# Performance work log

Hardware: AMD Instinct MI355X
Metric: run time of the kernel (lower is better)

Reference implementation:

```python
import jax, jax.numpy as jnp
import numpy as np

DIM = 4096
N_HEADS = 32
N_KV_HEADS = 8
HEAD_DIM = DIM // N_HEADS  # 128
N_REP = N_HEADS // N_KV_HEADS  # 4
FFN_HIDDEN = 11008
EPS = 1e-6
B, S = 4, 2048


def rms_norm(x, gamma):
    # x: [b, s, d]
    var = jnp.mean(x * x, axis=-1, keepdims=True)
    return gamma * (x * jax.lax.rsqrt(var + EPS))


def apply_rope(x, cos, sin):
    # x: [b, s, h, d]; cos/sin: [s, d/2]. Complex rotation on (even, odd) pairs.
    x2 = x.reshape(*x.shape[:-1], HEAD_DIM // 2, 2)
    x0, x1 = x2[..., 0], x2[..., 1]
    c = cos[None, :, None, :]
    s = sin[None, :, None, :]
    r0 = x0 * c - x1 * s
    r1 = x0 * s + x1 * c
    return jnp.stack([r0, r1], axis=-1).reshape(x.shape)


def setup_inputs() -> dict:
    key = jax.random.key(0)
    ks = jax.random.split(key, 16)
    sc = 0.02
    inp = {
        "x": jax.random.normal(ks[0], (B, S, DIM), dtype=jnp.float32),
        "freqs": jax.random.uniform(ks[1], (S, HEAD_DIM // 2), dtype=jnp.float32) * (2 * np.pi),
        "start_pos": 0,
        "gamma_attn": jnp.ones((DIM,), jnp.float32),
        "gamma_ffn": jnp.ones((DIM,), jnp.float32),
        "wq_w": sc * jax.random.normal(ks[2], (N_HEADS * HEAD_DIM, DIM), jnp.float32),
        "wq_b": jnp.zeros((N_HEADS * HEAD_DIM,), jnp.float32),
        "wk_w": sc * jax.random.normal(ks[3], (N_KV_HEADS * HEAD_DIM, DIM), jnp.float32),
        "wk_b": jnp.zeros((N_KV_HEADS * HEAD_DIM,), jnp.float32),
        "wv_w": sc * jax.random.normal(ks[4], (N_KV_HEADS * HEAD_DIM, DIM), jnp.float32),
        "wv_b": jnp.zeros((N_KV_HEADS * HEAD_DIM,), jnp.float32),
        "wo_w": sc * jax.random.normal(ks[5], (DIM, N_HEADS * HEAD_DIM), jnp.float32),
        "wo_b": jnp.zeros((DIM,), jnp.float32),
        "w1_w": sc * jax.random.normal(ks[6], (FFN_HIDDEN, DIM), jnp.float32),
        "w3_w": sc * jax.random.normal(ks[7], (FFN_HIDDEN, DIM), jnp.float32),
        "w2_w": sc * jax.random.normal(ks[8], (DIM, FFN_HIDDEN), jnp.float32),
    }
    return inp


def reference(x, freqs, start_pos, gamma_attn, gamma_ffn,
              wq_w, wq_b, wk_w, wk_b, wv_w, wv_b, wo_w, wo_b,
              w1_w, w3_w, w2_w):
    cos, sin = jnp.cos(freqs), jnp.sin(freqs)

    # --- attention sublayer ---
    xn = rms_norm(x, gamma_attn)
    xq = (xn @ wq_w.T + wq_b).reshape(B, S, N_HEADS, HEAD_DIM)
    xk = (xn @ wk_w.T + wk_b).reshape(B, S, N_KV_HEADS, HEAD_DIM)
    xv = (xn @ wv_w.T + wv_b).reshape(B, S, N_KV_HEADS, HEAD_DIM)
    xq = apply_rope(xq, cos, sin)
    xk = apply_rope(xk, cos, sin)

    # KV cache: start_pos=0 prefill -> cache slice [0:start_pos+S] == current xk/xv
    keys = jnp.repeat(xk, N_REP, axis=2)   # [b, s, n_heads, d]
    values = jnp.repeat(xv, N_REP, axis=2)

    scores = jnp.einsum('bqhd,bkhd->bhqk', xq, keys) / np.sqrt(HEAD_DIM)
    probs = jax.nn.softmax(scores.astype(jnp.float32), axis=-1).astype(xq.dtype)
    attn = jnp.einsum('bhqk,bkhd->bqhd', probs, values).reshape(B, S, DIM)
    h = x + attn @ wo_w.T + wo_b

    # --- FFN sublayer (LLaMA SwiGLU) ---
    hn = rms_norm(h, gamma_ffn)
    ff = (jax.nn.silu(hn @ w1_w.T) * (hn @ w3_w.T)) @ w2_w.T
    return h + ff
```

## Files before the change

### kernel.cpp

```cpp
#include <hip/hip_runtime.h>
#include <hip/hip_bf16.h>

#define DIM   4096
#define NH    32
#define NKV   8
#define HD    128
#define FFNH  11008
#define BATCH 4
#define SEQ   2048
#define MTOT  (BATCH*SEQ)

using bf16x8_t = __attribute__((ext_vector_type(8))) short;
using f32x4_t  = __attribute__((ext_vector_type(4))) float;

typedef const __attribute__((address_space(1))) unsigned int GlbU32;
typedef __attribute__((address_space(3))) unsigned int LdsU32;

__device__ __forceinline__ unsigned short f2b(float f) {
  union { float f; unsigned int u; } v; v.f = f;
  return (unsigned short)((v.u + 0x7fffu + ((v.u >> 16) & 1u)) >> 16);
}
__device__ __forceinline__ float b2f(unsigned short b) {
  union { unsigned int u; float f; } v; v.u = ((unsigned int)b) << 16;
  return v.f;
}
__device__ __forceinline__ void gll16(const void* g, void* l) {
  __builtin_amdgcn_global_load_lds((GlbU32*)g, (LdsU32*)l, 16, 0, 0);
}

#define VM8  asm volatile("s_waitcnt vmcnt(8)" ::: "memory")
#define VM4M asm volatile("s_waitcnt vmcnt(4)" ::: "memory")
#define VM0  asm volatile("s_waitcnt vmcnt(0)" ::: "memory")

__global__ __launch_bounds__(256)
void cvt_bf16_k(const float* __restrict__ src, unsigned short* __restrict__ dst)
{
  const size_t i = ((size_t)blockIdx.x * 256 + threadIdx.x) * 8;
  const float4 a = *(const float4*)&src[i];
  const float4 b = *(const float4*)&src[i + 4];
  union { int4 v; unsigned short u[8]; } o;
  o.u[0] = f2b(a.x); o.u[1] = f2b(a.y); o.u[2] = f2b(a.z); o.u[3] = f2b(a.w);
  o.u[4] = f2b(b.x); o.u[5] = f2b(b.y); o.u[6] = f2b(b.z); o.u[7] = f2b(b.w);
  *(int4*)&dst[i] = o.v;
}

__global__ __launch_bounds__(256)
void rmsnorm_k(const float* __restrict__ X, const float* __restrict__ gamma,
               unsigned short* __restrict__ Y)
{
  const int row = blockIdx.x, t = threadIdx.x;
  const float* xr = X + (size_t)row * DIM;
  float4 v[4];
  float ss = 0.f;
#pragma unroll
  for (int p = 0; p < 4; ++p) {
    v[p] = *(const float4*)&xr[p * 1024 + t * 4];
    ss += v[p].x*v[p].x + v[p].y*v[p].y + v[p].z*v[p].z + v[p].w*v[p].w;
  }
#pragma unroll
  for (int off = 32; off >= 1; off >>= 1) ss += __shfl_xor(ss, off, 64);
  __shared__ float red[4];
  if ((t & 63) == 0) red[t >> 6] = ss;
  __syncthreads();
  const float tot = red[0] + red[1] + red[2] + red[3];
  const float rn = rsqrtf(tot * (1.f / DIM) + 1e-6f);
  unsigned short* yr = Y + (size_t)row * DIM;
#pragma unroll
  for (int p = 0; p < 4; ++p) {
    const float4 gv = *(const float4*)&gamma[p * 1024 + t * 4];
    short4 o;
    o.x = (short)f2b(v[p].x * gv.x * rn);
    o.y = (short)f2b(v[p].y * gv.y * rn);
    o.z = (short)f2b(v[p].z * gv.z * rn);
    o.w = (short)f2b(v[p].w * gv.w * rn);
    *(short4*)&yr[p * 1024 + t * 4] = o;
  }
}

template<int NHT>
__global__ __launch_bounds__(256)
void rope_k(unsigned short* __restrict__ buf, const float* __restrict__ fr)
{
  const int u = blockIdx.x * 256 + threadIdx.x;
  const int per_row = NHT * 16;
  const int row  = u / per_row;
  const int rem  = u - row * per_row;
  const int head = rem >> 4;
  const int i4   = (rem & 15) << 2;
  const int s    = row & (SEQ - 1);
  unsigned short* p = buf + (size_t)row * (NHT * HD) + head * HD + i4 * 2;
  union { int4 v; unsigned short u16[8]; } d;
  d.v = *(const int4*)p;
  const float4 f = *(const float4*)&fr[s * 64 + i4];
  const float fa[4] = {f.x, f.y, f.z, f.w};
#pragma unroll
  for (int i = 0; i < 4; ++i) {
    float sn, c;
    __sincosf(fa[i], &sn, &c);
    const float x0 = b2f(d.u16[2*i]), x1 = b2f(d.u16[2*i+1]);
    d.u16[2*i]   = f2b(x0 * c - x1 * sn);
    d.u16[2*i+1] = f2b(x0 * sn + x1 * c);
  }
  *(int4*)p = d.v;
}

#define GP0(SLOT, STG, VM) {                                              \
  _Pragma("unroll") for (int n_ = 0; n_ < 4; ++n_) bf[n_] = rdB((SLOT), n_); \
  _Pragma("unroll") for (int m_ = 0; m_ < 4; ++m_) af[m_] = rdA((SLOT), m_ * 16); \
  STG;                                                                    \
  __builtin_amdgcn_s_barrier();                                           \
  asm volatile("s_waitcnt lgkmcnt(0)" ::: "memory");                      \
  __builtin_amdgcn_sched_barrier(0);                                      \
  __builtin_amdgcn_s_setprio(1);                                          \
  _Pragma("unroll") for (int m_ = 0; m_ < 4; ++m_)                        \
    _Pragma("unroll") for (int n_ = 0; n_ < 4; ++n_)                      \
      acc[m_][n_] = __builtin_amdgcn_mfma_f32_16x16x32_bf16(af[m_], bf[n_], acc[m_][n_], 0, 0, 0); \
  __builtin_amdgcn_s_setprio(0);                                          \
  VM;                                                                     \
  __builtin_amdgcn_s_barrier();                                           \
  __builtin_amdgcn_sched_barrier(0);                                      \
}
#define GP1(SLOT, STG, VM) {                                              \
  _Pragma("unroll") for (int m_ = 0; m_ < 4; ++m_) af[m_] = rdA((SLOT), 64 + m_ * 16); \
  STG;                                                                    \
  __builtin_amdgcn_s_barrier();                                           \
  asm volatile("s_waitcnt lgkmcnt(0)" ::: "memory");                      \
  __builtin_amdgcn_sched_barrier(0);                                      \
  __builtin_amdgcn_s_setprio(1);                                          \
  _Pragma("unroll") for (int m_ = 0; m_ < 4; ++m_)                        \
    _Pragma("unroll") for (int n_ = 0; n_ < 4; ++n_)                      \
      acc[4 + m_][n_] = __builtin_amdgcn_mfma_f32_16x16x32_bf16(af[m_], bf[n_], acc[4 + m_][n_], 0, 0, 0); \
  __builtin_amdgcn_s_setprio(0);                                          \
  VM;                                                                     \
  __builtin_amdgcn_s_barrier();                                           \
  __builtin_amdgcn_sched_barrier(0);                                      \
}

template<int MODE>
__global__ __launch_bounds__(512)
void gemm256(const unsigned short* __restrict__ A,
             const unsigned short* __restrict__ W,
             const unsigned short* __restrict__ W3p,
             const float* __restrict__ bias,
             const float* res,
             float* outF,
             unsigned short* __restrict__ outH,
             const unsigned short* __restrict__ wkp,
             const unsigned short* __restrict__ wvp,
             const float* __restrict__ bkp,
             const float* __restrict__ bvp,
             unsigned short* __restrict__ okp,
             unsigned short* __restrict__ ovp,
             int K)
{
  __shared__ __align__(16) char smem[131072];
  const int t = threadIdx.x, lane = t & 63, wid = t >> 6;
  const int wr = wid >> 2, wc = wid & 3;
  const int G = gridDim.x, bid = blockIdx.x;
  const int wg = (bid & 7) * (G >> 3) + (bid >> 3);
  const int NBN = G >> 5;
  const int span = NBN << 3;
  const int tmg = wg / span, rr = wg - tmg * span;
  const int tn = rr >> 3, tm = (tmg << 3) + (rr & 7);
  const int m0 = tm << 8;
  const int NT = K >> 6, NSUB = K >> 5;

  const unsigned short *P1, *P2;
  const float* bp = bias;
  unsigned short* oh = outH;
  int nloc = 0, colsN = 4096;
  if constexpr (MODE == 0) {
    const int n0 = tn << 8;
    if (n0 < 4096)      { nloc = n0;        P1 = W   + (size_t)nloc * K; bp = bias; oh = outH; colsN = 4096; }
    else if (n0 < 5120) { nloc = n0 - 4096; P1 = wkp + (size_t)nloc * K; bp = bkp;  oh = okp;  colsN = 1024; }
    else                { nloc = n0 - 5120; P1 = wvp + (size_t)nloc * K; bp = bvp;  oh = ovp;  colsN = 1024; }
    P2 = P1 + (size_t)128 * K;
  } else if constexpr (MODE == 3) {
    const int n0w = tn << 7;
    P1 = W   + (size_t)n0w * K;
    P2 = W3p + (size_t)n0w * K;
    nloc = n0w;
  } else {
    const int n0 = tn << 8;
    P1 = W + (size_t)n0 * K;
    P2 = P1 + (size_t)128 * K;
    nloc = n0;
  }

  const int r0 = t >> 2, gg = t & 3;
  const int gsw = gg ^ ((r0 >> 1) & 3);

  auto stA = [&](int sig) {
    if (sig < NSUB) {
      const int slot = sig & 3;
      gll16(A + (size_t)(m0 + r0) * K + sig * 32 + gsw * 8,
            smem + slot * 16384 + wid * 1024);
      gll16(A + (size_t)(m0 + 128 + r0) * K + sig * 32 + gsw * 8,
            smem + slot * 16384 + 8192 + wid * 1024);
    }
  };
  auto stB = [&](int sig) {
    if (sig < NSUB) {
      const int slot = sig & 3;
      gll16(P1 + (size_t)r0 * K + sig * 32 + gsw * 8,
            smem + 65536 + slot * 16384 + wid * 1024);
      gll16(P2 + (size_t)r0 * K + sig * 32 + gsw * 8,
            smem + 65536 + slot * 16384 + 8192 + wid * 1024);
    }
  };
  auto rdA = [&](int slot, int mo) -> bf16x8_t {
    const int lrow = wr * 128 + mo + (lane & 15);
    const int g = (lane >> 4) ^ ((lrow >> 1) & 3);
    return *(const bf16x8_t*)(smem + slot * 16384 + lrow * 64 + g * 16);
  };
  auto rdB = [&](int slot, int nf) -> bf16x8_t {
    const int brow = wc * 64 + nf * 16 + (lane & 15);
    const int g = (lane >> 4) ^ ((brow >> 1) & 3);
    return *(const bf16x8_t*)(smem + 65536 + slot * 16384 + brow * 64 + g * 16);
  };

  f32x4_t acc[8][4];
#pragma unroll
  for (int i = 0; i < 8; ++i)
#pragma unroll
    for (int j = 0; j < 4; ++j) acc[i][j] = (f32x4_t)0.f;
  bf16x8_t af[4], bf[4];

  stA(0); stB(0); stA(1); stB(1); stA(2); stB(2);
  VM8;
  __builtin_amdgcn_s_barrier();
  __builtin_amdgcn_sched_barrier(0);

  for (int kt = 0; kt < NT; ++kt) {
    const int slot0 = (2 * kt) & 3;
    const int slot1 = slot0 + 1;
    GP0(slot0, stA(2 * kt + 3), (void)0);
    GP1(slot0, stB(2 * kt + 3), if (kt < NT - 1) { VM8; } else { VM0; });
    GP0(slot1, stA(2 * kt + 4), (void)0);
    GP1(slot1, stB(2 * kt + 4), if (kt < NT - 2) { VM8; } else { VM4M; });
  }

  if constexpr (MODE == 0) {
#pragma unroll
    for (int ni = 0; ni < 4; ++ni) {
      const int col = nloc + wc * 64 + ni * 16 + (lane & 15);
      const float bv = bp[col];
#pragma unroll
      for (int mi = 0; mi < 8; ++mi)
#pragma unroll
        for (int r = 0; r < 4; ++r) {
          const int row = m0 + wr * 128 + mi * 16 + (lane >> 4) * 4 + r;
          oh[(size_t)row * colsN + col] = f2b(acc[mi][ni][r] + bv);
        }
    }
  } else if constexpr (MODE == 1 || MODE == 2) {
#pragma unroll
    for (int ni = 0; ni < 4; ++ni) {
      const int col = nloc + wc * 64 + ni * 16 + (lane & 15);
      float bv = 0.f;
      if constexpr (MODE == 1) bv = bias[col];
#pragma unroll
      for (int mi = 0; mi < 8; ++mi)
#pragma unroll
        for (int r = 0; r < 4; ++r) {
          const int row = m0 + wr * 128 + mi * 16 + (lane >> 4) * 4 + r;
          const size_t idx = (size_t)row * 4096 + col;
          outF[idx] = acc[mi][ni][r] + bv + res[idx];
        }
    }
  } else {
    if (wc >= 2) {
      const int widx = wr * 2 + (wc - 2);
#pragma unroll
      for (int ni = 0; ni < 4; ++ni)
#pragma unroll
        for (int mi = 0; mi < 8; ++mi)
#pragma unroll
          for (int r = 0; r < 4; ++r) {
            const int lrow = mi * 16 + (lane >> 4) * 4 + r;
            const int ncol = ni * 16 + (lane & 15);
            *(unsigned short*)(smem + widx * 16384 + lrow * 128 + ncol * 2) =
                f2b(acc[mi][ni][r]);
          }
    }
    __syncthreads();
    if (wc < 2) {
      const int widx = wr * 2 + wc;
#pragma unroll
      for (int ni = 0; ni < 4; ++ni)
#pragma unroll
        for (int mi = 0; mi < 8; ++mi)
#pragma unroll
          for (int r = 0; r < 4; ++r) {
            const int lrow = mi * 16 + (lane >> 4) * 4 + r;
            const int ncol = ni * 16 + (lane & 15);
            const float s3 = b2f(*(const unsigned short*)(smem + widx * 16384 + lrow * 128 + ncol * 2));
            const float s1 = acc[mi][ni][r];
            const float sig = 1.f / (1.f + __expf(-s1));
            const int row = m0 + wr * 128 + lrow;
            outH[(size_t)row * FFNH + nloc + wc * 64 + ncol] = f2b(s1 * sig * s3);
          }
    }
  }
}

__global__ __launch_bounds__(256)
void attn_k(const unsigned short* __restrict__ Q, const unsigned short* __restrict__ Kb,
            const unsigned short* __restrict__ Vb, unsigned short* __restrict__ O)
{
  __shared__ unsigned short Qs[8192];
  __shared__ unsigned short Ks[2][4096];
  __shared__ unsigned short Vt[2][4096];
  __shared__ unsigned short Ps[2048];
  const int t = threadIdx.x, lane = t & 63, wid = t >> 6;
  const int bx = blockIdx.x;
  const int qt = bx & 31, h = (bx >> 5) & 31, b = bx >> 10;
  const int kvh = h >> 2;
  const float rs = 0.08838834764831845f;

#pragma unroll
  for (int oo = 0; oo < 4; ++oo) {
    const int o = wid * 4 + oo;
    const int row = o * 4 + (lane >> 4);
    const int gl  = (lane & 15) ^ (row & 7);
    gll16(Q + (size_t)(b * SEQ + qt * 64 + row) * DIM + h * HD + gl * 8, &Qs[o * 512]);
  }

  const unsigned short* Kbase = Kb + (size_t)(b * SEQ) * (NKV * HD) + kvh * HD;
  const unsigned short* Vbase = Vb + (size_t)(b * SEQ) * (NKV * HD) + kvh * HD;

  auto stK = [&](int kt, int slot) {
#pragma unroll
    for (int oo = 0; oo < 2; ++oo) {
      const int o = wid * 2 + oo;
      const int row = o * 4 + (lane >> 4);
      const int gl  = (lane & 15) ^ (row & 7);
      gll16(Kbase + (size_t)(kt * 32 + row) * (NKV * HD) + gl * 8, &Ks[slot][o * 512]);
    }
  };
  const int kv = t >> 3, dc = (t & 7) << 4;
  const int colv = kv ^ ((t & 3) << 3);
  auto ldV = [&](int kt, int4& lo, int4& hi) {
    const unsigned short* gp = Vbase + (size_t)(kt * 32 + kv) * (NKV * HD) + dc;
    lo = *(const int4*)gp;
    hi = *(const int4*)(gp + 8);
  };

  int4 vlo0, vhi0, vlo1, vhi1;
  stK(0, 0); ldV(0, vlo0, vhi0);
  stK(1, 1); ldV(1, vlo1, vhi1);

  f32x4_t oa[8];
#pragma unroll
  for (int i = 0; i < 8; ++i) oa[i] = (f32x4_t)0.f;
  float mrun[4] = {-1e30f, -1e30f, -1e30f, -1e30f};
  float lrun[4] = {0.f, 0.f, 0.f, 0.f};
  const int q0 = wid * 16;

  auto iter = [&](int kt, int cur, int4& vlo, int4& vhi) {
    asm volatile("s_waitcnt vmcnt(4)" ::: "memory");
    {
      union { int4 v; unsigned short u[8]; } lo, hi;
      lo.v = vlo; hi.v = vhi;
#pragma unroll
      for (int j = 0; j < 8; ++j) Vt[cur][(dc + j) * 32 + colv] = lo.u[j];
#pragma unroll
      for (int j = 0; j < 8; ++j) Vt[cur][(dc + 8 + j) * 32 + colv] = hi.u[j];
    }
    asm volatile("s_waitcnt lgkmcnt(0)" ::: "memory");
    __builtin_amdgcn_sched_barrier(0);
    __builtin_amdgcn_s_barrier();
    __builtin_amdgcn_sched_barrier(0);

    f32x4_t sa0 = (f32x4_t)0.f, sa1 = (f32x4_t)0.f;
    const int arow = q0 + (lane & 15);
    const int kr0 = lane & 15, kr1 = 16 + (lane & 15);
#pragma unroll
    for (int ks = 0; ks < 4; ++ks) {
      const bf16x8_t aq  = *(const bf16x8_t*)&Qs[(arow * 128 + ks * 32 + (lane >> 4) * 8) ^ ((arow & 7) << 3)];
      const bf16x8_t bk0 = *(const bf16x8_t*)&Ks[cur][(kr0 * 128 + ks * 32 + (lane >> 4) * 8) ^ ((kr0 & 7) << 3)];
      sa0 = __builtin_amdgcn_mfma_f32_16x16x32_bf16(aq, bk0, sa0, 0, 0, 0);
      const bf16x8_t bk1 = *(const bf16x8_t*)&Ks[cur][(kr1 * 128 + ks * 32 + (lane >> 4) * 8) ^ ((kr1 & 7) << 3)];
      sa1 = __builtin_amdgcn_mfma_f32_16x16x32_bf16(aq, bk1, sa1, 0, 0, 0);
    }
    float pm[4];
#pragma unroll
    for (int r = 0; r < 4; ++r) {
      float v = fmaxf(sa0[r], sa1[r]) * rs;
#pragma unroll
      for (int off = 1; off < 16; off <<= 1) v = fmaxf(v, __shfl_xor(v, off, 64));
      pm[r] = v;
    }
    float corr[4], mnew[4];
#pragma unroll
    for (int r = 0; r < 4; ++r) {
      mnew[r] = fmaxf(mrun[r], pm[r]);
      corr[r] = __expf(mrun[r] - mnew[r]);
      mrun[r] = mnew[r];
    }
    float pv0[4], pv1[4];
#pragma unroll
    for (int r = 0; r < 4; ++r) {
      pv0[r] = __expf(sa0[r] * rs - mnew[r]);
      pv1[r] = __expf(sa1[r] * rs - mnew[r]);
    }
#pragma unroll
    for (int r = 0; r < 4; ++r) {
      float v = pv0[r] + pv1[r];
#pragma unroll
      for (int off = 1; off < 16; off <<= 1) v += __shfl_xor(v, off, 64);
      lrun[r] = lrun[r] * corr[r] + v;
    }
#pragma unroll
    for (int i = 0; i < 8; ++i)
#pragma unroll
      for (int r = 0; r < 4; ++r) oa[i][r] *= corr[r];

#pragma unroll
    for (int r = 0; r < 4; ++r) {
      Ps[wid * 512 + ((lane >> 4) * 4 + r) * 32 + (lane & 15)]      = f2b(pv0[r]);
      Ps[wid * 512 + ((lane >> 4) * 4 + r) * 32 + 16 + (lane & 15)] = f2b(pv1[r]);
    }
    const bf16x8_t pf = *(const bf16x8_t*)&Ps[wid * 512 + (lane & 15) * 32 + (lane >> 4) * 8];

#pragma unroll
    for (int nt2 = 0; nt2 < 8; ++nt2) {
      const bf16x8_t vf = *(const bf16x8_t*)&Vt[cur][(nt2 * 16 + (lane & 15)) * 32 + (((lane >> 4) ^ (nt2 & 3)) << 3)];
      oa[nt2] = __builtin_amdgcn_mfma_f32_16x16x32_bf16(pf, vf, oa[nt2], 0, 0, 0);
    }
    __builtin_amdgcn_s_barrier();
    __builtin_amdgcn_sched_barrier(0);
    if (kt + 2 < SEQ / 32) { stK(kt + 2, cur); ldV(kt + 2, vlo, vhi); }
  };

  for (int kt2 = 0; kt2 < SEQ / 32; kt2 += 2) {
    iter(kt2,     0, vlo0, vhi0);
    iter(kt2 + 1, 1, vlo1, vhi1);
  }

  float inv[4];
#pragma unroll
  for (int r = 0; r < 4; ++r) inv[r] = 1.f / lrun[r];
#pragma unroll
  for (int nt2 = 0; nt2 < 8; ++nt2) {
    const int col = h * HD + nt2 * 16 + (lane & 15);
#pragma unroll
    for (int r = 0; r < 4; ++r) {
      const int row = qt * 64 + q0 + (lane >> 4) * 4 + r;
      O[(size_t)(b * SEQ + row) * DIM + col] = f2b(oa[nt2][r] * inv[r]);
    }
  }
}

extern "C" void kernel_launch(void* const* d_in, const int* in_sizes, int n_in,
                              void* d_out, int out_size, void* d_ws, size_t ws_size,
                              hipStream_t stream)
{
  (void)in_sizes; (void)n_in; (void)out_size; (void)ws_size;
  const float* x   = (const float*)d_in[0];
  const float* fr  = (const float*)d_in[1];
  const float* ga  = (const float*)d_in[3];
  const float* gf  = (const float*)d_in[4];
  const float* wq  = (const float*)d_in[5];
  const float* wqb = (const float*)d_in[6];
  const float* wk  = (const float*)d_in[7];
  const float* wkb = (const float*)d_in[8];
  const float* wv  = (const float*)d_in[9];
  const float* wvb = (const float*)d_in[10];
  const float* wo  = (const float*)d_in[11];
  const float* wob = (const float*)d_in[12];
  const float* w1  = (const float*)d_in[13];
  const float* w3  = (const float*)d_in[14];
  const float* w2  = (const float*)d_in[15];
  float* out = (float*)d_out;

  constexpr size_t MB = 1ull << 20;
  char* ws = (char*)d_ws;
  unsigned short* xn = (unsigned short*)(ws);
  unsigned short* qb = (unsigned short*)(ws + 64*MB);
  unsigned short* kb = (unsigned short*)(ws + 128*MB);
  unsigned short* vb = (unsigned short*)(ws + 144*MB);
  unsigned short* ao = (unsigned short*)(ws + 160*MB);
  unsigned short* hn = (unsigned short*)(ws + 224*MB);
  unsigned short* g  = (unsigned short*)(ws);
  unsigned short* wscr = (unsigned short*)(ws + 288*MB);
  unsigned short* wqB = wscr;
  unsigned short* wkB = wscr + 16*MB;
  unsigned short* wvB = wscr + 20*MB;
  unsigned short* woB = wscr;
  unsigned short* w1B = wscr;
  unsigned short* w3B = wscr + 45*MB;
  unsigned short* w2B = wscr;

  rmsnorm_k<<<MTOT, 256, 0, stream>>>(x, ga, xn);
  cvt_bf16_k<<<(NH*HD*DIM)/2048,  256, 0, stream>>>(wq, wqB);
  cvt_bf16_k<<<(NKV*HD*DIM)/2048, 256, 0, stream>>>(wk, wkB);
  cvt_bf16_k<<<(NKV*HD*DIM)/2048, 256, 0, stream>>>(wv, wvB);
  gemm256<0><<<(MTOT/256)*((DIM+2*NKV*HD)/256), 512, 0, stream>>>(
      xn, wqB, nullptr, wqb, nullptr, nullptr, qb,
      wkB, wvB, wkb, wvb, kb, vb, DIM);
  rope_k<NH><<<(MTOT*NH*16)/256,  256, 0, stream>>>(qb, fr);
  rope_k<NKV><<<(MTOT*NKV*16)/256,256, 0, stream>>>(kb, fr);
  attn_k<<<BATCH*NH*(SEQ/64), 256, 0, stream>>>(qb, kb, vb, ao);
  cvt_bf16_k<<<(DIM*DIM)/2048, 256, 0, stream>>>(wo, woB);
  gemm256<1><<<(MTOT/256)*(DIM/256), 512, 0, stream>>>(
      ao, woB, nullptr, wob, x, out, nullptr,
      nullptr, nullptr, nullptr, nullptr, nullptr, nullptr, DIM);
  rmsnorm_k<<<MTOT, 256, 0, stream>>>(out, gf, hn);
  cvt_bf16_k<<<(FFNH*DIM)/2048, 256, 0, stream>>>(w1, w1B);
  cvt_bf16_k<<<(FFNH*DIM)/2048, 256, 0, stream>>>(w3, w3B);
  gemm256<3><<<(MTOT/256)*(FFNH/128), 512, 0, stream>>>(
      hn, w1B, w3B, nullptr, nullptr, nullptr, g,
      nullptr, nullptr, nullptr, nullptr, nullptr, nullptr, DIM);
  cvt_bf16_k<<<(FFNH*DIM)/2048, 256, 0, stream>>>(w2, w2B);
  gemm256<2><<<(MTOT/256)*(DIM/256), 512, 0, stream>>>(
      g, w2B, nullptr, nullptr, out, out, nullptr,
      nullptr, nullptr, nullptr, nullptr, nullptr, nullptr, FFNH);
}
```

Before: 4.029 ms.

## Restructure GEMM main loop into single-stage k-steps and process 64 keys per attention step

The GEMM main loop drops the two-phase GP0/GP1 macros and their sched_barriers. Each 32-wide k slice now loads all eight A fragments and four B fragments, issues the next stage's loads, and runs 32 MFMAs with one barrier. The attention kernel processes two 32-key tiles per iteration, which halves barriers and softmax reductions, and skips the running-max rescale when no row maximum grows. The costs are higher register pressure (eight A fragments, four score accumulators) and less overlap, because the loop now waits for all V loads with VM0 before the LDS writes.

After: 3.821 ms. 1.05x faster.

```diff
diff --git a/kernel.cpp b/kernel.cpp
--- a/kernel.cpp
+++ b/kernel.cpp
@@ -102,38 +102,6 @@
     d.u16[2*i+1] = f2b(x0 * sn + x1 * c);
   }
   *(int4*)p = d.v;
-}
-
-#define GP0(SLOT, STG, VM) {                                              \
-  _Pragma("unroll") for (int n_ = 0; n_ < 4; ++n_) bf[n_] = rdB((SLOT), n_); \
-  _Pragma("unroll") for (int m_ = 0; m_ < 4; ++m_) af[m_] = rdA((SLOT), m_ * 16); \
-  STG;                                                                    \
-  __builtin_amdgcn_s_barrier();                                           \
-  asm volatile("s_waitcnt lgkmcnt(0)" ::: "memory");                      \
-  __builtin_amdgcn_sched_barrier(0);                                      \
-  __builtin_amdgcn_s_setprio(1);                                          \
-  _Pragma("unroll") for (int m_ = 0; m_ < 4; ++m_)                        \
-    _Pragma("unroll") for (int n_ = 0; n_ < 4; ++n_)                      \
-      acc[m_][n_] = __builtin_amdgcn_mfma_f32_16x16x32_bf16(af[m_], bf[n_], acc[m_][n_], 0, 0, 0); \
-  __builtin_amdgcn_s_setprio(0);                                          \
-  VM;                                                                     \
-  __builtin_amdgcn_s_barrier();                                           \
-  __builtin_amdgcn_sched_barrier(0);                                      \
-}
-#define GP1(SLOT, STG, VM) {                                              \
-  _Pragma("unroll") for (int m_ = 0; m_ < 4; ++m_) af[m_] = rdA((SLOT), 64 + m_ * 16); \
-  STG;                                                                    \
-  __builtin_amdgcn_s_barrier();                                           \
-  asm volatile("s_waitcnt lgkmcnt(0)" ::: "memory");                      \
-  __builtin_amdgcn_sched_barrier(0);                                      \
-  __builtin_amdgcn_s_setprio(1);                                          \
-  _Pragma("unroll") for (int m_ = 0; m_ < 4; ++m_)                        \
-    _Pragma("unroll") for (int n_ = 0; n_ < 4; ++n_)                      \
-      acc[4 + m_][n_] = __builtin_amdgcn_mfma_f32_16x16x32_bf16(af[m_], bf[n_], acc[4 + m_][n_], 0, 0, 0); \
-  __builtin_amdgcn_s_setprio(0);                                          \
-  VM;                                                                     \
-  __builtin_amdgcn_s_barrier();                                           \
-  __builtin_amdgcn_sched_barrier(0);                                      \
 }
 
 template<int MODE>
@@ -163,7 +131,7 @@
   const int tmg = wg / span, rr = wg - tmg * span;
   const int tn = rr >> 3, tm = (tmg << 3) + (rr & 7);
   const int m0 = tm << 8;
-  const int NT = K >> 6, NSUB = K >> 5;
+  const int NSUB = K >> 5;
 
   const unsigned short *P1, *P2;
   const float* bp = bias;
@@ -224,20 +192,30 @@
   for (int i = 0; i < 8; ++i)
 #pragma unroll
     for (int j = 0; j < 4; ++j) acc[i][j] = (f32x4_t)0.f;
-  bf16x8_t af[4], bf[4];
 
   stA(0); stB(0); stA(1); stB(1); stA(2); stB(2);
   VM8;
   __builtin_amdgcn_s_barrier();
-  __builtin_amdgcn_sched_barrier(0);
-
-  for (int kt = 0; kt < NT; ++kt) {
-    const int slot0 = (2 * kt) & 3;
-    const int slot1 = slot0 + 1;
-    GP0(slot0, stA(2 * kt + 3), (void)0);
-    GP1(slot0, stB(2 * kt + 3), if (kt < NT - 1) { VM8; } else { VM0; });
-    GP0(slot1, stA(2 * kt + 4), (void)0);
-    GP1(slot1, stB(2 * kt + 4), if (kt < NT - 2) { VM8; } else { VM4M; });
+
+  for (int p = 0; p < NSUB; ++p) {
+    const int slot = p & 3;
+    bf16x8_t bfv[4], afv[8];
+#pragma unroll
+    for (int n = 0; n < 4; ++n) bfv[n] = rdB(slot, n);
+#pragma unroll
+    for (int m = 0; m < 8; ++m) afv[m] = rdA(slot, m * 16);
+    stA(p + 3); stB(p + 3);
+    __builtin_amdgcn_s_setprio(1);
+#pragma unroll
+    for (int m = 0; m < 8; ++m)
+#pragma unroll
+      for (int n = 0; n < 4; ++n)
+        acc[m][n] = __builtin_amdgcn_mfma_f32_16x16x32_bf16(afv[m], bfv[n], acc[m][n], 0, 0, 0);
+    __builtin_amdgcn_s_setprio(0);
+    if (p < NSUB - 3)      { VM8; }
+    else if (p == NSUB - 3){ VM4M; }
+    else                   { VM0; }
+    __builtin_amdgcn_s_barrier();
   }
 
   if constexpr (MODE == 0) {
@@ -311,7 +289,7 @@
   __shared__ unsigned short Qs[8192];
   __shared__ unsigned short Ks[2][4096];
   __shared__ unsigned short Vt[2][4096];
-  __shared__ unsigned short Ps[2048];
+  __shared__ unsigned short Ps[2][2048];
   const int t = threadIdx.x, lane = t & 63, wid = t >> 6;
   const int bx = blockIdx.x;
   const int qt = bx & 31, h = (bx >> 5) & 31, b = bx >> 10;
@@ -345,6 +323,14 @@
     lo = *(const int4*)gp;
     hi = *(const int4*)(gp + 8);
   };
+  auto wrV = [&](int slot, int4 vlo, int4 vhi) {
+    union { int4 v; unsigned short u[8]; } lo, hi;
+    lo.v = vlo; hi.v = vhi;
+#pragma unroll
+    for (int j = 0; j < 8; ++j) Vt[slot][(dc + j) * 32 + colv] = lo.u[j];
+#pragma unroll
+    for (int j = 0; j < 8; ++j) Vt[slot][(dc + 8 + j) * 32 + colv] = hi.u[j];
+  };
 
   int4 vlo0, vhi0, vlo1, vhi1;
   stK(0, 0); ldV(0, vlo0, vhi0);
@@ -357,85 +343,90 @@
   float lrun[4] = {0.f, 0.f, 0.f, 0.f};
   const int q0 = wid * 16;
 
-  auto iter = [&](int kt, int cur, int4& vlo, int4& vhi) {
-    asm volatile("s_waitcnt vmcnt(4)" ::: "memory");
-    {
-      union { int4 v; unsigned short u[8]; } lo, hi;
-      lo.v = vlo; hi.v = vhi;
-#pragma unroll
-      for (int j = 0; j < 8; ++j) Vt[cur][(dc + j) * 32 + colv] = lo.u[j];
-#pragma unroll
-      for (int j = 0; j < 8; ++j) Vt[cur][(dc + 8 + j) * 32 + colv] = hi.u[j];
-    }
+  for (int kp = 0; kp < SEQ / 64; ++kp) {
+    VM0;
+    wrV(0, vlo0, vhi0);
+    wrV(1, vlo1, vhi1);
     asm volatile("s_waitcnt lgkmcnt(0)" ::: "memory");
-    __builtin_amdgcn_sched_barrier(0);
     __builtin_amdgcn_s_barrier();
-    __builtin_amdgcn_sched_barrier(0);
 
     f32x4_t sa0 = (f32x4_t)0.f, sa1 = (f32x4_t)0.f;
+    f32x4_t sa2 = (f32x4_t)0.f, sa3 = (f32x4_t)0.f;
     const int arow = q0 + (lane & 15);
     const int kr0 = lane & 15, kr1 = 16 + (lane & 15);
 #pragma unroll
     for (int ks = 0; ks < 4; ++ks) {
       const bf16x8_t aq  = *(const bf16x8_t*)&Qs[(arow * 128 + ks * 32 + (lane >> 4) * 8) ^ ((arow & 7) << 3)];
-      const bf16x8_t bk0 = *(const bf16x8_t*)&Ks[cur][(kr0 * 128 + ks * 32 + (lane >> 4) * 8) ^ ((kr0 & 7) << 3)];
-      sa0 = __builtin_amdgcn_mfma_f32_16x16x32_bf16(aq, bk0, sa0, 0, 0, 0);
-      const bf16x8_t bk1 = *(const bf16x8_t*)&Ks[cur][(kr1 * 128 + ks * 32 + (lane >> 4) * 8) ^ ((kr1 & 7) << 3)];
-      sa1 = __builtin_amdgcn_mfma_f32_16x16x32_bf16(aq, bk1, sa1, 0, 0, 0);
-    }
+      const bf16x8_t b00 = *(const bf16x8_t*)&Ks[0][(kr0 * 128 + ks * 32 + (lane >> 4) * 8) ^ ((kr0 & 7) << 3)];
+      sa0 = __builtin_amdgcn_mfma_f32_16x16x32_bf16(aq, b00, sa0, 0, 0, 0);
+      const bf16x8_t b01 = *(const bf16x8_t*)&Ks[0][(kr1 * 128 + ks * 32 + (lane >> 4) * 8) ^ ((kr1 & 7) << 3)];
+      sa1 = __builtin_amdgcn_mfma_f32_16x16x32_bf16(aq, b01, sa1, 0, 0, 0);
+      const bf16x8_t b10 = *(const bf16x8_t*)&Ks[1][(kr0 * 128 + ks * 32 + (lane >> 4) * 8) ^ ((kr0 & 7) << 3)];
+      sa2 = __builtin_amdgcn_mfma_f32_16x16x32_bf16(aq, b10, sa2, 0, 0, 0);
+      const bf16x8_t b11 = *(const bf16x8_t*)&Ks[1][(kr1 * 128 + ks * 32 + (lane >> 4) * 8) ^ ((kr1 & 7) << 3)];
+      sa3 = __builtin_amdgcn_mfma_f32_16x16x32_bf16(aq, b11, sa3, 0, 0, 0);
+    }
+
     float pm[4];
 #pragma unroll
     for (int r = 0; r < 4; ++r) {
-      float v = fmaxf(sa0[r], sa1[r]) * rs;
+      float v = fmaxf(fmaxf(sa0[r], sa1[r]), fmaxf(sa2[r], sa3[r])) * rs;
 #pragma unroll
       for (int off = 1; off < 16; off <<= 1) v = fmaxf(v, __shfl_xor(v, off, 64));
       pm[r] = v;
     }
-    float corr[4], mnew[4];
+    const int grow = __any(pm[0] > mrun[0] || pm[1] > mrun[1] ||
+                           pm[2] > mrun[2] || pm[3] > mrun[3]);
+    if (grow) {
+#pragma unroll
+      for (int r = 0; r < 4; ++r) {
+        const float mnew = fmaxf(mrun[r], pm[r]);
+        const float corr = __expf(mrun[r] - mnew);
+        mrun[r] = mnew;
+        lrun[r] *= corr;
+#pragma unroll
+        for (int i = 0; i < 8; ++i) oa[i][r] *= corr;
+      }
+    }
+    float pv0[4], pv1[4], pv2[4], pv3[4];
 #pragma unroll
     for (int r = 0; r < 4; ++r) {
-      mnew[r] = fmaxf(mrun[r], pm[r]);
-      corr[r] = __expf(mrun[r] - mnew[r]);
-      mrun[r] = mnew[r];
-    }
-    float pv0[4], pv1[4];
+      pv0[r] = __expf(sa0[r] * rs - mrun[r]);
+      pv1[r] = __expf(sa1[r] * rs - mrun[r]);
+      pv2[r] = __expf(sa2[r] * rs - mrun[r]);
+      pv3[r] = __expf(sa3[r] * rs - mrun[r]);
+    }
 #pragma unroll
     for (int r = 0; r < 4; ++r) {
-      pv0[r] = __expf(sa0[r] * rs - mnew[r]);
-      pv1[r] = __expf(sa1[r] * rs - mnew[r]);
-    }
+      float v = pv0[r] + pv1[r] + pv2[r] + pv3[r];
+#pragma unroll
+      for (int off = 1; off < 16; off <<= 1) v += __shfl_xor(v, off, 64);
+      lrun[r] += v;
+    }
+
 #pragma unroll
     for (int r = 0; r < 4; ++r) {
-      float v = pv0[r] + pv1[r];
-#pragma unroll
-      for (int off = 1; off < 16; off <<= 1) v += __shfl_xor(v, off, 64);
-      lrun[r] = lrun[r] * corr[r] + v;
-    }
-#pragma unroll
-    for (int i = 0; i < 8; ++i)
-#pragma unroll
-      for (int r = 0; r < 4; ++r) oa[i][r] *= corr[r];
-
-#pragma unroll
-    for (int r = 0; r < 4; ++r) {
-      Ps[wid * 512 + ((lane >> 4) * 4 + r) * 32 + (lane & 15)]      = f2b(pv0[r]);
-      Ps[wid * 512 + ((lane >> 4) * 4 + r) * 32 + 16 + (lane & 15)] = f2b(pv1[r]);
-    }
-    const bf16x8_t pf = *(const bf16x8_t*)&Ps[wid * 512 + (lane & 15) * 32 + (lane >> 4) * 8];
+      const int prow = (lane >> 4) * 4 + r;
+      Ps[0][wid * 512 + prow * 32 + (lane & 15)]      = f2b(pv0[r]);
+      Ps[0][wid * 512 + prow * 32 + 16 + (lane & 15)] = f2b(pv1[r]);
+      Ps[1][wid * 512 + prow * 32 + (lane & 15)]      = f2b(pv2[r]);
+      Ps[1][wid * 512 + prow * 32 + 16 + (lane & 15)] = f2b(pv3[r]);
+    }
+    const bf16x8_t pf0 = *(const bf16x8_t*)&Ps[0][wid * 512 + (lane & 15) * 32 + (lane >> 4) * 8];
+    const bf16x8_t pf1 = *(const bf16x8_t*)&Ps[1][wid * 512 + (lane & 15) * 32 + (lane >> 4) * 8];
 
 #pragma unroll
     for (int nt2 = 0; nt2 < 8; ++nt2) {
-      const bf16x8_t vf = *(const bf16x8_t*)&Vt[cur][(nt2 * 16 + (lane & 15)) * 32 + (((lane >> 4) ^ (nt2 & 3)) << 3)];
-      oa[nt2] = __builtin_amdgcn_mfma_f32_16x16x32_bf16(pf, vf, oa[nt2], 0, 0, 0);
+      const bf16x8_t vf0 = *(const bf16x8_t*)&Vt[0][(nt2 * 16 + (lane & 15)) * 32 + (((lane >> 4) ^ (nt2 & 3)) << 3)];
+      oa[nt2] = __builtin_amdgcn_mfma_f32_16x16x32_bf16(pf0, vf0, oa[nt2], 0, 0, 0);
+      const bf16x8_t vf1 = *(const bf16x8_t*)&Vt[1][(nt2 * 16 + (lane & 15)) * 32 + (((lane >> 4) ^ (nt2 & 3)) << 3)];
+      oa[nt2] = __builtin_amdgcn_mfma_f32_16x16x32_bf16(pf1, vf1, oa[nt2], 0, 0, 0);
     }
     __builtin_amdgcn_s_barrier();
-    __builtin_amdgcn_sched_barrier(0);
-    if (kt + 2 < SEQ / 32) { stK(kt + 2, cur); ldV(kt + 2, vlo, vhi); }
-  };
-
-  for (int kt2 = 0; kt2 < SEQ / 32; kt2 += 2) {
-    iter(kt2,     0, vlo0, vhi0);
-    iter(kt2 + 1, 1, vlo1, vhi1);
+    if (kp + 1 < SEQ / 64) {
+      stK(2 * kp + 2, 0); ldV(2 * kp + 2, vlo0, vhi0);
+      stK(2 * kp + 3, 1); ldV(2 * kp + 3, vlo1, vhi1);
+    }
   }
 
   float inv[4];
```
